# Kernel tuning notes

Measured on AMD Instinct MI355X. Metric: run time of the kernel, lower is better.

Reference implementation:

```python
import jax, jax.numpy as jnp
import numpy as np

NH = 4        # n_head
L_TOPK = 16   # AWG top-k l
DEC = 2       # dec_layers
EPS = 1e-6


def _ln(x, g, b):
    m = jnp.mean(x, -1, keepdims=True)
    v = jnp.mean((x - m) ** 2, -1, keepdims=True)
    return (x - m) * jax.lax.rsqrt(v + EPS) * g + b


def _heads(x, W):
    B, L, C = x.shape
    return (x @ W).reshape(B, L, NH, C // NH).transpose(0, 2, 1, 3)  # [B,H,L,dk]


def _softmax_attn(qh, kh):
    dk = qh.shape[-1]
    logits = jnp.einsum('bhqd,bhkd->bhqk', qh / jnp.sqrt(jnp.float32(dk)), kh)
    return jax.nn.softmax(logits, axis=-1)


def cross_attn_block(q, k, v, Wq, Wk, Wv, Wo, g, b):
    B, Lq, C = q.shape
    a = _softmax_attn(_heads(q, Wq), _heads(k, Wk))
    o = jnp.einsum('bhqk,bhkd->bhqd', a, _heads(v, Wv))
    o = o.transpose(0, 2, 1, 3).reshape(B, Lq, C) @ Wo
    return _ln(o + q, g, b)


def awg_attn_block(q, k, v, Wq, Wk, Wv, Wo, g, b):
    # top-k attention-weight-gating: keep weights >= l-th largest, renormalize
    B, Lq, C = q.shape
    a = _softmax_attn(_heads(q, Wq), _heads(k, Wk))
    thr = jax.lax.top_k(a, L_TOPK)[0][..., -1:]          # [B,H,Lq,1]
    w = a * (a >= thr).astype(a.dtype)
    w = w / jnp.sum(w, -1, keepdims=True)
    o = jnp.einsum('bhqk,bhkd->bhqd', w, _heads(v, Wv))
    o = o.transpose(0, 2, 1, 3).reshape(B, Lq, C) @ Wo
    return _ln(o + q, g, b)


def setup_inputs() -> dict:
    key = jax.random.key(0)
    ks = jax.random.split(key, 32)
    B, Lq, Lk, C, F = 4, 3000, 750, 64, 256
    s = 1.0 / np.sqrt(C)
    sf = 1.0 / np.sqrt(F)
    d = {}
    d['q'] = jax.random.normal(ks[0], (B, Lq, C), jnp.float32)
    d['enc'] = jax.random.normal(ks[1], (B, Lk, C), jnp.float32)
    # cross_attn_layer params
    for i, n in enumerate(['cal_Wq', 'cal_Wk', 'cal_Wv', 'cal_Wo']):
        d[n] = jax.random.normal(ks[2 + i], (C, C), jnp.float32) * s
    d['cal_ln1_g'] = jnp.ones((C,), jnp.float32)
    d['cal_ln1_b'] = jnp.zeros((C,), jnp.float32)
    d['cal_W1'] = jax.random.normal(ks[6], (C, F), jnp.float32) * s
    d['cal_b1'] = jnp.zeros((F,), jnp.float32)
    d['cal_W2'] = jax.random.normal(ks[7], (F, C), jnp.float32) * sf
    d['cal_b2'] = jnp.zeros((C,), jnp.float32)
    d['cal_ln2_g'] = jnp.ones((C,), jnp.float32)
    d['cal_ln2_b'] = jnp.zeros((C,), jnp.float32)
    # stacked MGAN params [DEC, ...]
    d['m_ln_g'] = jnp.ones((DEC, C), jnp.float32)
    d['m_ln_b'] = jnp.zeros((DEC, C), jnp.float32)
    d['m_fc1_W'] = jax.random.normal(ks[8], (DEC, C, C), jnp.float32) * s
    d['m_fc1_b'] = jnp.zeros((DEC, C), jnp.float32)
    d['m_fc2_W'] = jax.random.normal(ks[9], (DEC, C, C), jnp.float32) * s
    d['m_fc2_b'] = jnp.zeros((DEC, C), jnp.float32)
    for i, n in enumerate(['m_Wq', 'm_Wk', 'm_Wv', 'm_Wo']):
        d[n] = jax.random.normal(ks[10 + i], (DEC, C, C), jnp.float32) * s
    d['m_aln_g'] = jnp.ones((DEC, C), jnp.float32)
    d['m_aln_b'] = jnp.zeros((DEC, C), jnp.float32)
    d['fc_W'] = jax.random.normal(ks[14], (C, 1), jnp.float32) * s
    d['fc_b'] = jnp.zeros((1,), jnp.float32)
    return d


def reference(q, enc, cal_Wq, cal_Wk, cal_Wv, cal_Wo, cal_ln1_g, cal_ln1_b,
              cal_W1, cal_b1, cal_W2, cal_b2, cal_ln2_g, cal_ln2_b,
              m_ln_g, m_ln_b, m_fc1_W, m_fc1_b, m_fc2_W, m_fc2_b,
              m_Wq, m_Wk, m_Wv, m_Wo, m_aln_g, m_aln_b, fc_W, fc_b):
    # cross_attn_layer: attention + FFN + LN (dropout = identity in eval)
    x = cross_attn_block(q, enc, enc, cal_Wq, cal_Wk, cal_Wv, cal_Wo, cal_ln1_g, cal_ln1_b)
    ffn = jax.nn.relu(x @ cal_W1 + cal_b1) @ cal_W2 + cal_b2
    x = _ln(ffn + x, cal_ln2_g, cal_ln2_b)
    # MGAN decoder layers (rep_KV: k,v = encoder output)
    for i in range(DEC):
        qn = _ln(x, m_ln_g[i], m_ln_b[i])
        sg = jax.nn.sigmoid(qn @ m_fc1_W[i] + m_fc1_b[i]) * (qn @ m_fc2_W[i] + m_fc2_b[i])
        awg = awg_attn_block(sg, enc, enc, m_Wq[i], m_Wk[i], m_Wv[i], m_Wo[i],
                             m_aln_g[i], m_aln_b[i])
        # GLU(cat(sg, awg)) = sg * sigmoid(awg)
        x = qn + sg * jax.nn.sigmoid(awg)
    # label_type='p' head
    return jax.nn.sigmoid(x @ fc_W + fc_b)  # [B, Lq, 1]
```

## Files before the change

### kernel.cpp

```cpp
#include <hip/hip_runtime.h>
#include <hip/hip_bf16.h>

using bf16 = __hip_bfloat16;

#define DEV_INLINE __device__ __forceinline__

constexpr int B_  = 4;
constexpr int LQ  = 3000;
constexpr int LK  = 750;
constexpr int NH_ = 4;
constexpr float EPSF = 1e-6f;

constexpr int PITCH = 753;

constexpr size_t WS_KV = 0;
constexpr size_t WS_XB = 1152000;
constexpr size_t WS_QP = 1920000;
constexpr size_t WS_AO = 2688000;
constexpr size_t WS_QN = 3456000;
constexpr size_t WS_SG = 4224000;

typedef _Float16 half2_t __attribute__((ext_vector_type(2)));
typedef _Float16 half4_t __attribute__((ext_vector_type(4)));
typedef float    f32x4   __attribute__((ext_vector_type(4)));

#define MFMA16(a, b, c) __builtin_amdgcn_mfma_f32_16x16x16f16((a), (b), (c), 0, 0, 0)

DEV_INLINE float sigmoidf(float x) { return 1.f / (1.f + __expf(-x)); }

DEV_INLINE unsigned int packh2(float a, float b) {
  half2_t h = { (_Float16)a, (_Float16)b };
  unsigned int u; __builtin_memcpy(&u, &h, 4); return u;
}
DEV_INLINE half2_t u2h(unsigned int u) {
  half2_t h; __builtin_memcpy(&h, &u, 4); return h;
}
DEV_INLINE unsigned short f2h(float f) {
  _Float16 h = (_Float16)f;
  unsigned short u; __builtin_memcpy(&u, &h, 2); return u;
}
DEV_INLINE half4_t h4_from(const unsigned short* p) {
  unsigned int lo = *(const unsigned int*)p;
  unsigned int hi = *(const unsigned int*)(p + 2);
  unsigned long long v = ((unsigned long long)hi << 32) | lo;
  half4_t h; __builtin_memcpy(&h, &v, 8); return h;
}
DEV_INLINE float dot2(unsigned int kw, half2_t qh, float acc) {
  return __builtin_amdgcn_fdot2(u2h(kw), qh, acc, false);
}

DEV_INLINE unsigned int f2sort(float f) {
  int ib = __float_as_int(f);
  return (unsigned int)(ib ^ ((ib >> 31) | 0x80000000));
}
DEV_INLINE float sort2f(unsigned int u) {
  const int ib = (u & 0x80000000u) ? (int)(u ^ 0x80000000u) : (int)~u;
  return __int_as_float(ib);
}

DEV_INLINE unsigned int bcastu(unsigned int v) {
  return (unsigned int)__builtin_amdgcn_readfirstlane((int)v);
}

DEV_INLINE void sort64u_desc4(unsigned int v[4]) {
  const int lane = threadIdx.x & 63;
  #pragma unroll
  for (int k = 2; k <= 64; k <<= 1) {
    #pragma unroll
    for (int j = k >> 1; j > 0; j >>= 1) {
      const bool takeMax = ((lane & j) == 0) == ((lane & k) == 0);
      #pragma unroll
      for (int r = 0; r < 4; ++r) {
        const unsigned int o = __shfl_xor(v[r], j);
        v[r] = (takeMax == (v[r] > o)) ? v[r] : o;
      }
    }
  }
}
DEV_INLINE void sort64p_desc4(unsigned long long v[4]) {
  const int lane = threadIdx.x & 63;
  #pragma unroll
  for (int k = 2; k <= 64; k <<= 1) {
    #pragma unroll
    for (int j = k >> 1; j > 0; j >>= 1) {
      const bool takeMax = ((lane & j) == 0) == ((lane & k) == 0);
      #pragma unroll
      for (int r = 0; r < 4; ++r) {
        const unsigned long long o = __shfl_xor(v[r], j);
        v[r] = (takeMax == (v[r] > o)) ? v[r] : o;
      }
    }
  }
}

DEV_INLINE float row_ln(float v, float g, float b) {
  float s1 = v, s2 = v * v;
  #pragma unroll
  for (int off = 32; off > 0; off >>= 1) {
    s1 += __shfl_xor(s1, off);
    s2 += __shfl_xor(s2, off);
  }
  const float m   = s1 * (1.f / 64.f);
  const float var = s2 * (1.f / 64.f) - m * m;
  return (v - m) * rsqrtf(var + EPSF) * g + b;
}

__global__ __launch_bounds__(256) void kvq_proj_kernel(
    const float* __restrict__ enc, const float* __restrict__ q,
    const float* __restrict__ calWq,
    const float* __restrict__ calWk, const float* __restrict__ calWv,
    const float* __restrict__ mWk, const float* __restrict__ mWv,
    float* __restrict__ kv, float* __restrict__ qp)
{
  const int y = blockIdx.y;
  if (y < 6 && blockIdx.x >= 188) return;
  __shared__ float Wl[64 * 65];
  __shared__ float xs[16][64];
  const int t = threadIdx.x, rr = t >> 6, cc = t & 63;
  const float* W;
  const float* src;
  float* dst;
  float scale = 1.f;
  int nrows = 3000;
  switch (y) {
    case 0: W = calWk; src = enc; dst = kv;               break;
    case 1: W = calWv; src = enc; dst = kv + 192000;      break;
    case 2: W = mWk;        src = enc; dst = kv + 384000; break;
    case 3: W = mWv;        src = enc; dst = kv + 576000; break;
    case 4: W = mWk + 4096; src = enc; dst = kv + 768000; break;
    case 5: W = mWv + 4096; src = enc; dst = kv + 960000; break;
    default: W = calWq; src = q; dst = qp; scale = 0.25f; nrows = 12000; break;
  }
  const bool packK = (y == 2) || (y == 4);
  for (int i = t; i < 4096; i += 256) Wl[(i >> 6) * 65 + (i & 63)] = W[i];
  const int base = blockIdx.x * 16;
  for (int i = t; i < 1024; i += 256) {
    const int grow = base + (i >> 6);
    xs[i >> 6][i & 63] = (grow < nrows) ? src[(size_t)grow * 64 + (i & 63)] : 0.f;
  }
  __syncthreads();
  #pragma unroll
  for (int p = 0; p < 4; ++p) {
    const int row = p * 4 + rr;
    const int grow = base + row;
    float acc = 0.f;
    #pragma unroll
    for (int c = 0; c < 64; ++c) acc = fmaf(xs[row][c], Wl[c * 65 + cc], acc);
    if (packK) {
      const float accN = __shfl_xor(acc, 1);
      if (!(cc & 1) && grow < nrows)
        ((unsigned int*)dst)[(size_t)grow * 32 + (cc >> 1)] = packh2(acc, accN);
    } else if (grow < nrows) {
      dst[(size_t)grow * 64 + cc] = acc * scale;
    }
  }
}

__global__ __launch_bounds__(256) void cross_attn_kernel(
    const float* __restrict__ qp, const float* __restrict__ kp,
    const float* __restrict__ vp, float* __restrict__ ao)
{
  extern __shared__ char smem[];
  unsigned short* Kl = (unsigned short*)smem;
  unsigned short* Vt = Kl + 750 * 18;
  unsigned short* Pt = Vt + 16 * 754;

  const int t = threadIdx.x;
  const int h = blockIdx.y, b = blockIdx.z;
  const float* kslab = kp + (size_t)(b * LK) * 64 + h * 16;
  const float* vslab = vp + (size_t)(b * LK) * 64 + h * 16;

  for (int k = t; k < LK; k += 256) {
    const float4* ks = (const float4*)(kslab + (size_t)k * 64);
    const float4* vs = (const float4*)(vslab + (size_t)k * 64);
    unsigned int* kr = (unsigned int*)(Kl + k * 18);
    #pragma unroll
    for (int q4 = 0; q4 < 4; ++q4) {
      float4 a = ks[q4], v = vs[q4];
      kr[q4 * 2]     = packh2(a.x, a.y);
      kr[q4 * 2 + 1] = packh2(a.z, a.w);
      Vt[(q4 * 4 + 0) * 754 + k] = f2h(v.x);
      Vt[(q4 * 4 + 1) * 754 + k] = f2h(v.y);
      Vt[(q4 * 4 + 2) * 754 + k] = f2h(v.z);
      Vt[(q4 * 4 + 3) * 754 + k] = f2h(v.w);
    }
  }
  if (t < 32) Vt[(t & 15) * 754 + 750 + (t >> 4)] = 0;
  __syncthreads();

  const int wave = t >> 6, lane = t & 63;
  const int col = lane & 15, quad = lane >> 4;
  const int qbase = blockIdx.x * 64 + wave * 16;
  unsigned short* Pt_w = Pt + wave * 288;

  int qrow = qbase + col; if (qrow >= LQ) qrow = LQ - 1;
  const float* qptr = qp + ((size_t)(b * LQ + qrow)) * 64 + h * 16 + quad * 4;
  half4_t aQ;
  {
    unsigned long long v = ((unsigned long long)packh2(qptr[2], qptr[3]) << 32)
                         | packh2(qptr[0], qptr[1]);
    __builtin_memcpy(&aQ, &v, 8);
  }

  f32x4 O = {0.f, 0.f, 0.f, 0.f};
  float Zp[4] = {0.f, 0.f, 0.f, 0.f};
  const f32x4 zeroC = {0.f, 0.f, 0.f, 0.f};

  for (int tile = 0; tile < 47; ++tile) {
    const int key = tile * 16 + col;
    const half4_t bK = h4_from(Kl + key * 18 + quad * 4);
    f32x4 S = MFMA16(aQ, bK, zeroC);
    const bool valid = key < LK;
    float e0 = valid ? __expf(S[0]) : 0.f;
    float e1 = valid ? __expf(S[1]) : 0.f;
    float e2 = valid ? __expf(S[2]) : 0.f;
    float e3 = valid ? __expf(S[3]) : 0.f;
    Zp[0] += e0; Zp[1] += e1; Zp[2] += e2; Zp[3] += e3;
    Pt_w[(quad * 4 + 0) * 18 + col] = f2h(e0);
    Pt_w[(quad * 4 + 1) * 18 + col] = f2h(e1);
    Pt_w[(quad * 4 + 2) * 18 + col] = f2h(e2);
    Pt_w[(quad * 4 + 3) * 18 + col] = f2h(e3);
    const half4_t aP = h4_from(Pt_w + col * 18 + quad * 4);
    const half4_t bV = h4_from(Vt + col * 754 + tile * 16 + quad * 4);
    O = MFMA16(aP, bV, O);
  }

  #pragma unroll
  for (int r = 0; r < 4; ++r) {
    float z = Zp[r];
    z += __shfl_xor(z, 1);
    z += __shfl_xor(z, 2);
    z += __shfl_xor(z, 4);
    z += __shfl_xor(z, 8);
    Zp[r] = z;
  }

  #pragma unroll
  for (int r = 0; r < 4; ++r) {
    const int orow = qbase + quad * 4 + r;
    if (orow < LQ)
      ao[((size_t)(b * LQ + orow)) * 64 + h * 16 + col] = O[r] / Zp[r];
  }
}

__global__ __launch_bounds__(512) void awg_attn_kernel(
    const float* __restrict__ qp, const unsigned int* __restrict__ kp,
    const float* __restrict__ vp, float* __restrict__ ao)
{
  extern __shared__ char smem[];
  uint2*              KT2  = (uint2*)smem;
  unsigned long long* cand = (unsigned long long*)(smem + 4 * PITCH * 8);
  float*              selW = (float*)(smem + 4 * PITCH * 8 + 16384);
  unsigned short*     selK = (unsigned short*)(smem + 4 * PITCH * 8 + 16384 + 3072);

  const int t = threadIdx.x;
  const int h = blockIdx.y, b = blockIdx.z;
  const unsigned int* kslab = kp + ((size_t)(b * LK)) * 32 + h * 8;

  for (int k = t; k < LK; k += 512) {
    const uint2* ks = (const uint2*)(kslab + (size_t)k * 32);
    #pragma unroll
    for (int d4 = 0; d4 < 4; ++d4) KT2[d4 * PITCH + k] = ks[d4];
  }
  __syncthreads();

  const int wave = t >> 6, lane = t & 63;
  const unsigned long long below = (1ull << lane) - 1ull;
  unsigned long long* cd = cand + wave * 256;
  float*              sW = selW + wave * 96;
  unsigned short*     sK = selK + wave * 96;

  sW[lane] = -3.0e38f; sK[lane] = 0;
  if (lane < 32) { sW[64 + lane] = -3.0e38f; sK[64 + lane] = 0; }
  #pragma unroll
  for (int r = 0; r < 4; ++r) cd[r * 64 + lane] = 0ull;

  const int r0 = blockIdx.x * 32 + wave * 4;
  int r0r = r0; if (r0r > LQ - 4) r0r = LQ - 4;
  const float* qrow = qp + ((size_t)(b * LQ + r0r)) * 64 + h * 16;
  unsigned int qw[4][8];
  #pragma unroll
  for (int r = 0; r < 4; ++r) {
    #pragma unroll
    for (int i = 0; i < 8; ++i)
      qw[r][i] = bcastu(packh2(qrow[r * 64 + 2 * i], qrow[r * 64 + 2 * i + 1]));
  }

  float lg[4][12];
  #pragma unroll
  for (int tt = 0; tt < 12; ++tt) {
    const int k = lane + (tt << 6);
    if (tt < 11 || k < LK) {
      float a0 = 0.f, a1 = 0.f, a2 = 0.f, a3 = 0.f;
      #pragma unroll
      for (int d4 = 0; d4 < 4; ++d4) {
        const uint2 w = KT2[d4 * PITCH + k];
        a0 = dot2(w.x, u2h(qw[0][2 * d4]), a0); a0 = dot2(w.y, u2h(qw[0][2 * d4 + 1]), a0);
        a1 = dot2(w.x, u2h(qw[1][2 * d4]), a1); a1 = dot2(w.y, u2h(qw[1][2 * d4 + 1]), a1);
        a2 = dot2(w.x, u2h(qw[2][2 * d4]), a2); a2 = dot2(w.y, u2h(qw[2][2 * d4 + 1]), a2);
        a3 = dot2(w.x, u2h(qw[3][2 * d4]), a3); a3 = dot2(w.y, u2h(qw[3][2 * d4 + 1]), a3);
      }
      lg[0][tt] = a0; lg[1][tt] = a1; lg[2][tt] = a2; lg[3][tt] = a3;
    } else {
      lg[0][tt] = -3.0e38f; lg[1][tt] = -3.0e38f;
      lg[2][tt] = -3.0e38f; lg[3][tt] = -3.0e38f;
    }
  }

  unsigned int hs[4];
  #pragma unroll
  for (int r = 0; r < 4; ++r) {
    float m = lg[r][0];
    #pragma unroll
    for (int tt = 1; tt < 12; ++tt) m = fmaxf(m, lg[r][tt]);
    hs[r] = f2sort(m);
  }

  sort64u_desc4(hs);
  unsigned int L[4];
  #pragma unroll
  for (int r = 0; r < 4; ++r) L[r] = __shfl(hs[r], 15);

  int cb[4] = {0, 0, 0, 0};
  #pragma unroll
  for (int tt = 0; tt < 12; ++tt) {
    const int k = lane + (tt << 6);
    #pragma unroll
    for (int r = 0; r < 4; ++r) {
      const unsigned int s = f2sort(lg[r][tt]);
      const bool p = s >= L[r];
      const unsigned long long m = __ballot(p);
      if (p) {
        const int pos = cb[r] + (int)__popcll(m & below);
        if (pos < 64)
          cd[r * 64 + pos] = ((unsigned long long)s << 16) | (unsigned int)k;
      }
      cb[r] += (int)__popcll(m);
    }
  }

  unsigned long long sv[4];
  #pragma unroll
  for (int r = 0; r < 4; ++r) sv[r] = cd[r * 64 + lane];
  sort64p_desc4(sv);

  unsigned int su[4], cu15[4];
  float Mv[4];
  #pragma unroll
  for (int r = 0; r < 4; ++r) {
    su[r]   = (unsigned int)(sv[r] >> 16);
    cu15[r] = __shfl(su[r], 15);
    Mv[r]   = sort2f(__shfl(su[r], 0));
  }
  #pragma unroll
  for (int r = 0; r < 4; ++r) {
    if (lane < 24 && su[r] >= cu15[r]) {
      sW[r * 24 + lane] = sort2f(su[r]);
      sK[r * 24 + lane] = (unsigned short)(sv[r] & 0xFFFFull);
    }
  }

  const int dd = lane & 15;
  const int rsel = lane >> 4;
  const float ref = (rsel == 0) ? Mv[0] : (rsel == 1) ? Mv[1] : (rsel == 2) ? Mv[2] : Mv[3];
  const float* cwr = sW + rsel * 24;
  const unsigned short* cir = sK + rsel * 24;
  const float* vbase = vp + (size_t)(b * LK) * 64 + h * 16 + dd;
  float acc = 0.f, Z = 0.f;
  #pragma unroll
  for (int j = 0; j < 24; ++j) {
    const float e = __expf(cwr[j] - ref);
    Z += e;
    acc = fmaf(e, vbase[(size_t)cir[j] * 64], acc);
  }
  if (r0 + rsel < LQ)
    ao[((size_t)(b * LQ + r0 + rsel)) * 64 + h * 16 + dd] = acc / Z;
}

__global__ __launch_bounds__(256) void cross_ffn_kernel(
    const float* __restrict__ ao, const float* __restrict__ qres,
    const float* __restrict__ Wo,
    const float* __restrict__ g1, const float* __restrict__ b1n,
    const float* __restrict__ W1, const float* __restrict__ bb1,
    const float* __restrict__ W2, const float* __restrict__ bb2,
    const float* __restrict__ g2, const float* __restrict__ b2n,
    float* __restrict__ xout)
{
  __shared__ float xs[8][64];
  __shared__ float hs[8][256];
  const int t = threadIdx.x, rr = t >> 6, cc = t & 63;
  const size_t base = (size_t)blockIdx.x * 8;
  for (int i = t; i < 512; i += 256) xs[i >> 6][i & 63] = ao[base * 64 + i];
  __syncthreads();
  float acc[2];
  #pragma unroll
  for (int p = 0; p < 2; ++p) {
    const int row = p * 4 + rr;
    float a = 0.f;
    #pragma unroll
    for (int c = 0; c < 64; ++c) a = fmaf(xs[row][c], Wo[c * 64 + cc], a);
    acc[p] = a + qres[(base + row) * 64 + cc];
  }
  __syncthreads();
  #pragma unroll
  for (int p = 0; p < 2; ++p) {
    const int row = p * 4 + rr;
    xs[row][cc] = row_ln(acc[p], g1[cc], b1n[cc]);
  }
  __syncthreads();
  {
    float hv[8];
    #pragma unroll
    for (int r = 0; r < 8; ++r) hv[r] = 0.f;
    #pragma unroll 8
    for (int c = 0; c < 64; ++c) {
      const float w = W1[c * 256 + t];
      #pragma unroll
      for (int r = 0; r < 8; ++r) hv[r] = fmaf(xs[r][c], w, hv[r]);
    }
    const float bb = bb1[t];
    #pragma unroll
    for (int r = 0; r < 8; ++r) hs[r][t] = fmaxf(hv[r] + bb, 0.f);
  }
  __syncthreads();
  float acc2[2];
  #pragma unroll
  for (int p = 0; p < 2; ++p) acc2[p] = bb2[cc];
  #pragma unroll 8
  for (int c = 0; c < 256; ++c) {
    const float w = W2[c * 64 + cc];
    acc2[0] = fmaf(hs[rr][c], w, acc2[0]);
    acc2[1] = fmaf(hs[4 + rr][c], w, acc2[1]);
  }
  #pragma unroll
  for (int p = 0; p < 2; ++p) {
    const int row = p * 4 + rr;
    const float a = acc2[p] + xs[row][cc];
    xout[(base + row) * 64 + cc] = row_ln(a, g2[cc], b2n[cc]);
  }
}

__global__ __launch_bounds__(256) void mgan_pre_kernel(
    const float* __restrict__ x, const float* __restrict__ lng,
    const float* __restrict__ lnb, const float* __restrict__ W1,
    const float* __restrict__ bb1, const float* __restrict__ W2,
    const float* __restrict__ bb2, const float* __restrict__ Wq,
    float* __restrict__ qn, float* __restrict__ sg, float* __restrict__ qp)
{
  __shared__ float qs[8][64];
  __shared__ float sgs[8][64];
  const int t = threadIdx.x, rr = t >> 6, cc = t & 63;
  const size_t base = (size_t)blockIdx.x * 8;
  #pragma unroll
  for (int p = 0; p < 2; ++p) {
    const int row = p * 4 + rr;
    const float v = x[(base + row) * 64 + cc];
    const float qv = row_ln(v, lng[cc], lnb[cc]);
    qn[(base + row) * 64 + cc] = qv;
    qs[row][cc] = qv;
  }
  __syncthreads();
  float d1[2], d2[2];
  #pragma unroll
  for (int p = 0; p < 2; ++p) { d1[p] = bb1[cc]; d2[p] = bb2[cc]; }
  #pragma unroll 4
  for (int c = 0; c < 64; ++c) {
    const float w1 = W1[c * 64 + cc];
    const float w2 = W2[c * 64 + cc];
    #pragma unroll
    for (int p = 0; p < 2; ++p) {
      const float xv = qs[p * 4 + rr][c];
      d1[p] = fmaf(xv, w1, d1[p]);
      d2[p] = fmaf(xv, w2, d2[p]);
    }
  }
  #pragma unroll
  for (int p = 0; p < 2; ++p) {
    const int row = p * 4 + rr;
    const float sv = sigmoidf(d1[p]) * d2[p];
    sg[(base + row) * 64 + cc] = sv;
    sgs[row][cc] = sv;
  }
  __syncthreads();
  #pragma unroll
  for (int p = 0; p < 2; ++p) {
    const int row = p * 4 + rr;
    float a = 0.f;
    #pragma unroll
    for (int c = 0; c < 64; ++c) a = fmaf(sgs[row][c], Wq[c * 64 + cc], a);
    qp[(base + row) * 64 + cc] = a * 0.25f;
  }
}

__global__ __launch_bounds__(256) void out_pre_kernel(
    const float* __restrict__ ao, const float* __restrict__ sg,
    const float* __restrict__ qn, const float* __restrict__ Wo,
    const float* __restrict__ g_, const float* __restrict__ b_,
    const float* __restrict__ lng, const float* __restrict__ lnb,
    const float* __restrict__ W1, const float* __restrict__ bb1,
    const float* __restrict__ W2, const float* __restrict__ bb2,
    const float* __restrict__ Wq,
    float* __restrict__ qn_out, float* __restrict__ sg_out,
    float* __restrict__ qp_out)
{
  __shared__ float xs[8][64];
  __shared__ float sgs[8][64];
  const int t = threadIdx.x, rr = t >> 6, cc = t & 63;
  const size_t base = (size_t)blockIdx.x * 8;
  for (int i = t; i < 512; i += 256) xs[i >> 6][i & 63] = ao[base * 64 + i];
  __syncthreads();
  float accp[2], sgv[2];
  #pragma unroll
  for (int p = 0; p < 2; ++p) {
    const int row = p * 4 + rr;
    const size_t idx = (base + row) * 64 + cc;
    float a = 0.f;
    #pragma unroll
    for (int c = 0; c < 64; ++c) a = fmaf(xs[row][c], Wo[c * 64 + cc], a);
    sgv[p] = sg[idx];
    accp[p] = a + sgv[p];
  }
  __syncthreads();
  #pragma unroll
  for (int p = 0; p < 2; ++p) {
    const int row = p * 4 + rr;
    const size_t idx = (base + row) * 64 + cc;
    const float awg = row_ln(accp[p], g_[cc], b_[cc]);
    const float xv = qn[idx] + sgv[p] * sigmoidf(awg);
    const float qv = row_ln(xv, lng[cc], lnb[cc]);
    qn_out[idx] = qv;
    xs[row][cc] = qv;
  }
  __syncthreads();
  float d1[2], d2[2];
  #pragma unroll
  for (int p = 0; p < 2; ++p) { d1[p] = bb1[cc]; d2[p] = bb2[cc]; }
  #pragma unroll 4
  for (int c = 0; c < 64; ++c) {
    const float w1 = W1[c * 64 + cc];
    const float w2 = W2[c * 64 + cc];
    #pragma unroll
    for (int p = 0; p < 2; ++p) {
      const float xv = xs[p * 4 + rr][c];
      d1[p] = fmaf(xv, w1, d1[p]);
      d2[p] = fmaf(xv, w2, d2[p]);
    }
  }
  __syncthreads();
  #pragma unroll
  for (int p = 0; p < 2; ++p) {
    const int row = p * 4 + rr;
    const size_t idx = (base + row) * 64 + cc;
    const float sv = sigmoidf(d1[p]) * d2[p];
    sg_out[idx] = sv;
    sgs[row][cc] = sv;
  }
  __syncthreads();
  #pragma unroll
  for (int p = 0; p < 2; ++p) {
    const int row = p * 4 + rr;
    float a = 0.f;
    #pragma unroll
    for (int c = 0; c < 64; ++c) a = fmaf(sgs[row][c], Wq[c * 64 + cc], a);
    qp_out[(base + row) * 64 + cc] = a * 0.25f;
  }
}

__global__ __launch_bounds__(256) void out_final_kernel(
    const float* __restrict__ ao, const float* __restrict__ sg,
    const float* __restrict__ qn, const float* __restrict__ Wo,
    const float* __restrict__ g_, const float* __restrict__ b_,
    const float* __restrict__ fw, const float* __restrict__ fb,
    float* __restrict__ out)
{
  __shared__ float xs[8][64];
  const int t = threadIdx.x, rr = t >> 6, cc = t & 63;
  const size_t base = (size_t)blockIdx.x * 8;
  for (int i = t; i < 512; i += 256) xs[i >> 6][i & 63] = ao[base * 64 + i];
  __syncthreads();
  #pragma unroll
  for (int p = 0; p < 2; ++p) {
    const int row = p * 4 + rr;
    const size_t idx = (base + row) * 64 + cc;
    float a = 0.f;
    #pragma unroll
    for (int c = 0; c < 64; ++c) a = fmaf(xs[row][c], Wo[c * 64 + cc], a);
    const float sgv = sg[idx];
    a += sgv;
    const float awg = row_ln(a, g_[cc], b_[cc]);
    const float xv = qn[idx] + sgv * sigmoidf(awg);
    float v = xv * fw[cc];
    #pragma unroll
    for (int off = 32; off > 0; off >>= 1) v += __shfl_xor(v, off);
    if (cc == 0) out[base + row] = sigmoidf(v + fb[0]);
  }
}

extern "C" void kernel_launch(void* const* d_in, const int* in_sizes, int n_in,
                              void* d_out, int out_size, void* d_ws, size_t ws_size,
                              hipStream_t stream) {
  (void)in_sizes; (void)n_in; (void)out_size; (void)ws_size;

  const float* q     = (const float*)d_in[0];
  const float* enc   = (const float*)d_in[1];
  const float* calWq = (const float*)d_in[2];
  const float* calWk = (const float*)d_in[3];
  const float* calWv = (const float*)d_in[4];
  const float* calWo = (const float*)d_in[5];
  const float* ln1g  = (const float*)d_in[6];
  const float* ln1b  = (const float*)d_in[7];
  const float* W1    = (const float*)d_in[8];
  const float* b1v   = (const float*)d_in[9];
  const float* W2    = (const float*)d_in[10];
  const float* b2v   = (const float*)d_in[11];
  const float* ln2g  = (const float*)d_in[12];
  const float* ln2b  = (const float*)d_in[13];
  const float* mlng  = (const float*)d_in[14];
  const float* mlnb  = (const float*)d_in[15];
  const float* mfc1W = (const float*)d_in[16];
  const float* mfc1b = (const float*)d_in[17];
  const float* mfc2W = (const float*)d_in[18];
  const float* mfc2b = (const float*)d_in[19];
  const float* mWq   = (const float*)d_in[20];
  const float* mWk   = (const float*)d_in[21];
  const float* mWv   = (const float*)d_in[22];
  const float* mWo   = (const float*)d_in[23];
  const float* malng = (const float*)d_in[24];
  const float* malnb = (const float*)d_in[25];
  const float* fcW   = (const float*)d_in[26];
  const float* fcb   = (const float*)d_in[27];
  float* out = (float*)d_out;

  float* ws  = (float*)d_ws;
  float* kv  = ws + WS_KV;
  float* qp  = ws + WS_QP;
  float* aob = ws + WS_AO;
  float* qnb = ws + WS_QN;
  float* sgb = ws + WS_SG;
  float* xb  = ws + WS_XB;

  const size_t crossLds = (750 * 18 + 16 * 754 + 4 * 288) * 2;
  const size_t awgLds   = 4 * PITCH * 8 + 16384 + 3072 + 1536;

  kvq_proj_kernel<<<dim3(750, 7), 256, 0, stream>>>(enc, q, calWq, calWk, calWv,
                                                    mWk, mWv, kv, qp);

  cross_attn_kernel<<<dim3(47, NH_, B_), 256, crossLds, stream>>>(qp, kv, kv + 192000, aob);
  cross_ffn_kernel<<<1500, 256, 0, stream>>>(aob, q, calWo, ln1g, ln1b,
                                             W1, b1v, W2, b2v, ln2g, ln2b, xb);

  mgan_pre_kernel<<<1500, 256, 0, stream>>>(xb, mlng, mlnb, mfc1W, mfc1b,
                                            mfc2W, mfc2b, mWq, qnb, sgb, qp);
  awg_attn_kernel<<<dim3(94, NH_, B_), 512, awgLds, stream>>>(
      qp, (const unsigned int*)(kv + 2 * 192000), kv + 3 * 192000, aob);
  out_pre_kernel<<<1500, 256, 0, stream>>>(aob, sgb, qnb, mWo, malng, malnb,
                                           mlng + 64, mlnb + 64,
                                           mfc1W + 4096, mfc1b + 64,
                                           mfc2W + 4096, mfc2b + 64,
                                           mWq + 4096, qnb, sgb, qp);

  awg_attn_kernel<<<dim3(94, NH_, B_), 512, awgLds, stream>>>(
      qp, (const unsigned int*)(kv + 4 * 192000), kv + 5 * 192000, aob);
  out_final_kernel<<<1500, 256, 0, stream>>>(aob, sgb, qnb, mWo + 4096,
                                             malng + 64, malnb + 64, fcW, fcb, out);
}
```

Baseline: 360.0 us.

## Fuse cross FFN with MGAN pre-stage and use 32-bit candidate sort in AWG

New measurement: 364.1 us. No clear change (+1.1%).

```diff
diff --git a/kernel.cpp b/kernel.cpp
--- a/kernel.cpp
+++ b/kernel.cpp
@@ -11,7 +11,7 @@
 constexpr int NH_ = 4;
 constexpr float EPSF = 1e-6f;
 
-constexpr int PITCH = 753;
+constexpr int PITCH = 751;
 
 constexpr size_t WS_KV = 0;
 constexpr size_t WS_XB = 1152000;
@@ -72,21 +72,6 @@
       #pragma unroll
       for (int r = 0; r < 4; ++r) {
         const unsigned int o = __shfl_xor(v[r], j);
-        v[r] = (takeMax == (v[r] > o)) ? v[r] : o;
-      }
-    }
-  }
-}
-DEV_INLINE void sort64p_desc4(unsigned long long v[4]) {
-  const int lane = threadIdx.x & 63;
-  #pragma unroll
-  for (int k = 2; k <= 64; k <<= 1) {
-    #pragma unroll
-    for (int j = k >> 1; j > 0; j >>= 1) {
-      const bool takeMax = ((lane & j) == 0) == ((lane & k) == 0);
-      #pragma unroll
-      for (int r = 0; r < 4; ++r) {
-        const unsigned long long o = __shfl_xor(v[r], j);
         v[r] = (takeMax == (v[r] > o)) ? v[r] : o;
       }
     }
@@ -248,10 +233,11 @@
     const float* __restrict__ vp, float* __restrict__ ao)
 {
   extern __shared__ char smem[];
-  uint2*              KT2  = (uint2*)smem;
-  unsigned long long* cand = (unsigned long long*)(smem + 4 * PITCH * 8);
-  float*              selW = (float*)(smem + 4 * PITCH * 8 + 16384);
-  unsigned short*     selK = (unsigned short*)(smem + 4 * PITCH * 8 + 16384 + 3072);
+  uint2*          KT2   = (uint2*)smem;
+  unsigned int*   candV = (unsigned int*)(smem + 4 * PITCH * 8);
+  unsigned short* candK = (unsigned short*)(smem + 4 * PITCH * 8 + 8192);
+  float*          selW  = (float*)(smem + 4 * PITCH * 8 + 8192 + 4096);
+  unsigned short* selK  = (unsigned short*)(smem + 4 * PITCH * 8 + 8192 + 4096 + 3072);
 
   const int t = threadIdx.x;
   const int h = blockIdx.y, b = blockIdx.z;
@@ -266,14 +252,15 @@
 
   const int wave = t >> 6, lane = t & 63;
   const unsigned long long below = (1ull << lane) - 1ull;
-  unsigned long long* cd = cand + wave * 256;
-  float*              sW = selW + wave * 96;
-  unsigned short*     sK = selK + wave * 96;
+  unsigned int*   cV = candV + wave * 256;
+  unsigned short* cK = candK + wave * 256;
+  float*          sW = selW + wave * 96;
+  unsigned short* sK = selK + wave * 96;
 
   sW[lane] = -3.0e38f; sK[lane] = 0;
   if (lane < 32) { sW[64 + lane] = -3.0e38f; sK[64 + lane] = 0; }
   #pragma unroll
-  for (int r = 0; r < 4; ++r) cd[r * 64 + lane] = 0ull;
+  for (int r = 0; r < 4; ++r) cV[r * 64 + lane] = 0u;
 
   const int r0 = blockIdx.x * 32 + wave * 4;
   int r0r = r0; if (r0r > LQ - 4) r0r = LQ - 4;
@@ -332,31 +319,30 @@
       const unsigned long long m = __ballot(p);
       if (p) {
         const int pos = cb[r] + (int)__popcll(m & below);
-        if (pos < 64)
-          cd[r * 64 + pos] = ((unsigned long long)s << 16) | (unsigned int)k;
+        if (pos < 64) { cV[r * 64 + pos] = s; cK[r * 64 + pos] = (unsigned short)k; }
       }
       cb[r] += (int)__popcll(m);
     }
   }
 
-  unsigned long long sv[4];
-  #pragma unroll
-  for (int r = 0; r < 4; ++r) sv[r] = cd[r * 64 + lane];
-  sort64p_desc4(sv);
-
-  unsigned int su[4], cu15[4];
-  float Mv[4];
+  unsigned int su[4], so[4];
+  #pragma unroll
+  for (int r = 0; r < 4; ++r) { su[r] = cV[r * 64 + lane]; so[r] = su[r]; }
+  sort64u_desc4(so);
+  unsigned int T[4]; float Mv[4];
   #pragma unroll
   for (int r = 0; r < 4; ++r) {
-    su[r]   = (unsigned int)(sv[r] >> 16);
-    cu15[r] = __shfl(su[r], 15);
-    Mv[r]   = sort2f(__shfl(su[r], 0));
-  }
+    T[r]  = __shfl(so[r], 15);
+    Mv[r] = sort2f(__shfl(so[r], 0));
+  }
+
   #pragma unroll
   for (int r = 0; r < 4; ++r) {
-    if (lane < 24 && su[r] >= cu15[r]) {
-      sW[r * 24 + lane] = sort2f(su[r]);
-      sK[r * 24 + lane] = (unsigned short)(sv[r] & 0xFFFFull);
+    const bool w = su[r] >= T[r];
+    const unsigned long long mw = __ballot(w);
+    if (w) {
+      const int pos = (int)__popcll(mw & below);
+      if (pos < 24) { sW[r * 24 + pos] = sort2f(su[r]); sK[r * 24 + pos] = cK[r * 64 + lane]; }
     }
   }
 
@@ -377,17 +363,21 @@
     ao[((size_t)(b * LQ + r0 + rsel)) * 64 + h * 16 + dd] = acc / Z;
 }
 
-__global__ __launch_bounds__(256) void cross_ffn_kernel(
+__global__ __launch_bounds__(256) void ffn_pre_kernel(
     const float* __restrict__ ao, const float* __restrict__ qres,
     const float* __restrict__ Wo,
     const float* __restrict__ g1, const float* __restrict__ b1n,
     const float* __restrict__ W1, const float* __restrict__ bb1,
     const float* __restrict__ W2, const float* __restrict__ bb2,
     const float* __restrict__ g2, const float* __restrict__ b2n,
-    float* __restrict__ xout)
+    const float* __restrict__ lng, const float* __restrict__ lnb,
+    const float* __restrict__ fc1W, const float* __restrict__ fc1b,
+    const float* __restrict__ fc2W, const float* __restrict__ fc2b,
+    const float* __restrict__ Wq,
+    float* __restrict__ qn, float* __restrict__ sg, float* __restrict__ qp)
 {
   __shared__ float xs[8][64];
-  __shared__ float hs[8][256];
+  __shared__ float hsm[8][256];
   const int t = threadIdx.x, rr = t >> 6, cc = t & 63;
   const size_t base = (size_t)blockIdx.x * 8;
   for (int i = t; i < 512; i += 256) xs[i >> 6][i & 63] = ao[base * 64 + i];
@@ -402,10 +392,11 @@
     acc[p] = a + qres[(base + row) * 64 + cc];
   }
   __syncthreads();
-  #pragma unroll
-  for (int p = 0; p < 2; ++p) {
-    const int row = p * 4 + rr;
-    xs[row][cc] = row_ln(acc[p], g1[cc], b1n[cc]);
+  float x1[2];
+  #pragma unroll
+  for (int p = 0; p < 2; ++p) {
+    x1[p] = row_ln(acc[p], g1[cc], b1n[cc]);
+    xs[p * 4 + rr][cc] = x1[p];
   }
   __syncthreads();
   {
@@ -420,7 +411,7 @@
     }
     const float bb = bb1[t];
     #pragma unroll
-    for (int r = 0; r < 8; ++r) hs[r][t] = fmaxf(hv[r] + bb, 0.f);
+    for (int r = 0; r < 8; ++r) hsm[r][t] = fmaxf(hv[r] + bb, 0.f);
   }
   __syncthreads();
   float acc2[2];
@@ -429,66 +420,53 @@
   #pragma unroll 8
   for (int c = 0; c < 256; ++c) {
     const float w = W2[c * 64 + cc];
-    acc2[0] = fmaf(hs[rr][c], w, acc2[0]);
-    acc2[1] = fmaf(hs[4 + rr][c], w, acc2[1]);
-  }
-  #pragma unroll
-  for (int p = 0; p < 2; ++p) {
-    const int row = p * 4 + rr;
-    const float a = acc2[p] + xs[row][cc];
-    xout[(base + row) * 64 + cc] = row_ln(a, g2[cc], b2n[cc]);
-  }
-}
-
-__global__ __launch_bounds__(256) void mgan_pre_kernel(
-    const float* __restrict__ x, const float* __restrict__ lng,
-    const float* __restrict__ lnb, const float* __restrict__ W1,
-    const float* __restrict__ bb1, const float* __restrict__ W2,
-    const float* __restrict__ bb2, const float* __restrict__ Wq,
-    float* __restrict__ qn, float* __restrict__ sg, float* __restrict__ qp)
-{
-  __shared__ float qs[8][64];
-  __shared__ float sgs[8][64];
-  const int t = threadIdx.x, rr = t >> 6, cc = t & 63;
-  const size_t base = (size_t)blockIdx.x * 8;
-  #pragma unroll
-  for (int p = 0; p < 2; ++p) {
-    const int row = p * 4 + rr;
-    const float v = x[(base + row) * 64 + cc];
-    const float qv = row_ln(v, lng[cc], lnb[cc]);
-    qn[(base + row) * 64 + cc] = qv;
-    qs[row][cc] = qv;
-  }
+    acc2[0] = fmaf(hsm[rr][c], w, acc2[0]);
+    acc2[1] = fmaf(hsm[4 + rr][c], w, acc2[1]);
+  }
+  float qv[2];
+  #pragma unroll
+  for (int p = 0; p < 2; ++p) {
+    const int row = p * 4 + rr;
+    const float xv = row_ln(acc2[p] + x1[p], g2[cc], b2n[cc]);
+    qv[p] = row_ln(xv, lng[cc], lnb[cc]);
+    qn[(base + row) * 64 + cc] = qv[p];
+  }
+  __syncthreads();
+  #pragma unroll
+  for (int p = 0; p < 2; ++p) xs[p * 4 + rr][cc] = qv[p];
   __syncthreads();
   float d1[2], d2[2];
   #pragma unroll
-  for (int p = 0; p < 2; ++p) { d1[p] = bb1[cc]; d2[p] = bb2[cc]; }
+  for (int p = 0; p < 2; ++p) { d1[p] = fc1b[cc]; d2[p] = fc2b[cc]; }
   #pragma unroll 4
   for (int c = 0; c < 64; ++c) {
-    const float w1 = W1[c * 64 + cc];
-    const float w2 = W2[c * 64 + cc];
+    const float w1 = fc1W[c * 64 + cc];
+    const float w2 = fc2W[c * 64 + cc];
     #pragma unroll
     for (int p = 0; p < 2; ++p) {
-      const float xv = qs[p * 4 + rr][c];
-      d1[p] = fmaf(xv, w1, d1[p]);
-      d2[p] = fmaf(xv, w2, d2[p]);
-    }
-  }
-  #pragma unroll
-  for (int p = 0; p < 2; ++p) {
-    const int row = p * 4 + rr;
-    const float sv = sigmoidf(d1[p]) * d2[p];
-    sg[(base + row) * 64 + cc] = sv;
-    sgs[row][cc] = sv;
-  }
-  __syncthreads();
-  #pragma unroll
-  for (int p = 0; p < 2; ++p) {
-    const int row = p * 4 + rr;
-    float a = 0.f;
-    #pragma unroll
-    for (int c = 0; c < 64; ++c) a = fmaf(sgs[row][c], Wq[c * 64 + cc], a);
-    qp[(base + row) * 64 + cc] = a * 0.25f;
+      const float xq = xs[p * 4 + rr][c];
+      d1[p] = fmaf(xq, w1, d1[p]);
+      d2[p] = fmaf(xq, w2, d2[p]);
+    }
+  }
+  float sv[2];
+  #pragma unroll
+  for (int p = 0; p < 2; ++p) {
+    const int row = p * 4 + rr;
+    sv[p] = sigmoidf(d1[p]) * d2[p];
+    sg[(base + row) * 64 + cc] = sv[p];
+  }
+  __syncthreads();
+  #pragma unroll
+  for (int p = 0; p < 2; ++p) xs[p * 4 + rr][cc] = sv[p];
+  __syncthreads();
+  #pragma unroll
+  for (int p = 0; p < 2; ++p) {
+    const int row = p * 4 + rr;
+    float aq = 0.f;
+    #pragma unroll
+    for (int c = 0; c < 64; ++c) aq = fmaf(xs[row][c], Wq[c * 64 + cc], aq);
+    qp[(base + row) * 64 + cc] = aq * 0.25f;
   }
 }
 
@@ -637,20 +615,19 @@
   float* aob = ws + WS_AO;
   float* qnb = ws + WS_QN;
   float* sgb = ws + WS_SG;
-  float* xb  = ws + WS_XB;
 
   const size_t crossLds = (750 * 18 + 16 * 754 + 4 * 288) * 2;
-  const size_t awgLds   = 4 * PITCH * 8 + 16384 + 3072 + 1536;
+  const size_t awgLds   = 4 * PITCH * 8 + 8192 + 4096 + 3072 + 1536;
 
   kvq_proj_kernel<<<dim3(750, 7), 256, 0, stream>>>(enc, q, calWq, calWk, calWv,
                                                     mWk, mWv, kv, qp);
 
   cross_attn_kernel<<<dim3(47, NH_, B_), 256, crossLds, stream>>>(qp, kv, kv + 192000, aob);
-  cross_ffn_kernel<<<1500, 256, 0, stream>>>(aob, q, calWo, ln1g, ln1b,
-                                             W1, b1v, W2, b2v, ln2g, ln2b, xb);
-
-  mgan_pre_kernel<<<1500, 256, 0, stream>>>(xb, mlng, mlnb, mfc1W, mfc1b,
-                                            mfc2W, mfc2b, mWq, qnb, sgb, qp);
+  ffn_pre_kernel<<<1500, 256, 0, stream>>>(aob, q, calWo, ln1g, ln1b,
+                                           W1, b1v, W2, b2v, ln2g, ln2b,
+                                           mlng, mlnb, mfc1W, mfc1b,
+                                           mfc2W, mfc2b, mWq, qnb, sgb, qp);
+
   awg_attn_kernel<<<dim3(94, NH_, B_), 512, awgLds, stream>>>(
       qp, (const unsigned int*)(kv + 2 * 192000), kv + 3 * 192000, aob);
   out_pre_kernel<<<1500, 256, 0, stream>>>(aob, sgb, qnb, mWo, malng, malnb,
```
